# Performance work log

Hardware: AMD Instinct MI355X
Metric: run time of the kernel (lower is better)

## Reference

```python
import jax, jax.numpy as jnp
import numpy as np

C = 256
GROUPS = 32
HEADS = 4
EPS = 1e-5

def setup_inputs() -> dict:
    key = jax.random.key(0)
    ks = jax.random.split(key, 6)
    N, H, W = 4, 64, 64
    s = 1.0 / np.sqrt(C)
    return {
        "x": jax.random.normal(ks[0], (N, C, H, W), dtype=jnp.float32),
        "gamma": jnp.ones((C,), jnp.float32),
        "beta": jnp.zeros((C,), jnp.float32),
        "Wq": jax.random.normal(ks[1], (C, C), jnp.float32) * s,
        "Wk": jax.random.normal(ks[2], (C, C), jnp.float32) * s,
        "Wv": jax.random.normal(ks[3], (C, C), jnp.float32) * s,
        "Wp": jax.random.normal(ks[4], (C, C), jnp.float32) * s,
        "bp": jnp.zeros((C,), jnp.float32),
    }

def group_norm(x, gamma, beta):
    N, Cc, H, W = x.shape
    xg = x.reshape(N, GROUPS, Cc // GROUPS, H, W)
    mean = jnp.mean(xg, axis=(2, 3, 4), keepdims=True)
    var = jnp.var(xg, axis=(2, 3, 4), keepdims=True)
    xg = (xg - mean) * jax.lax.rsqrt(var + EPS)
    x = xg.reshape(N, Cc, H, W)
    return x * gamma[None, :, None, None] + beta[None, :, None, None]

def reference(x, gamma, beta, Wq, Wk, Wv, Wp, bp):
    N, Cc, H, W = x.shape
    dh = Cc // HEADS
    L = H * W
    xn = group_norm(x, gamma, beta)           # [N,C,H,W]
    xf = xn.reshape(N, Cc, L)                 # [N,C,L]
    # 1x1 convs == channel matmuls; split into heads: [N,heads,L,dh]
    def proj_heads(Wm):
        t = jnp.einsum('oc,ncl->nol', Wm, xf)
        return t.reshape(N, HEADS, dh, L).transpose(0, 1, 3, 2)
    q = proj_heads(Wq)
    k = proj_heads(Wk)
    v = proj_heads(Wv)
    scale = dh ** -0.5
    attn = jnp.einsum('nhld,nhmd->nhlm', q, k) * scale  # [N,heads,L,L]
    attn = jax.nn.softmax(attn, axis=-1)
    out = jnp.einsum('nhlm,nhmd->nhld', attn, v)        # [N,heads,L,dh]
    out = out.transpose(0, 1, 3, 2).reshape(N, Cc, L)   # [N,C,L]
    out = jnp.einsum('oc,ncl->nol', Wp, out) + bp[None, :, None]
    return out.reshape(N, Cc, H, W)
```

## Files before the change

kernel.cpp:

```cpp
#include <hip/hip_runtime.h>
#include <cstddef>
#include <cstdint>

#define NB 4
#define CC 256
#define LL 4096
#define NG 32
#define CPG 8
#define NH 4
#define DH 64
#define PSPLIT 4194304

static constexpr float EPSV  = 1e-5f;
static constexpr float SCALE_Q = 0.125f * 1.4426950408889634f;

typedef __attribute__((ext_vector_type(8))) short bf16x8;
typedef __attribute__((ext_vector_type(4))) float f32x4;
typedef _Float16 f16x8 __attribute__((ext_vector_type(8)));
typedef _Float16 f16x4 __attribute__((ext_vector_type(4)));
typedef __fp16  h16x2 __attribute__((ext_vector_type(2)));

__device__ __forceinline__ short f2bf(float f) {
  unsigned u = __float_as_uint(f);
  unsigned r = (u + 0x7fffu + ((u >> 16) & 1u)) >> 16;
  return (short)r;
}
__device__ __forceinline__ short f2h(float f) {
  union { _Float16 h; short s; } u;
  u.h = (_Float16)f;
  return u.s;
}
__device__ __forceinline__ int sw(int row, int chunk) {
  return row * 64 + ((chunk ^ (row & 7)) * 8);
}

__global__ __launch_bounds__(256) void gnstats_wcvt(
    const float* __restrict__ x, float* __restrict__ pstat,
    const float* __restrict__ Wq, const float* __restrict__ Wk,
    const float* __restrict__ Wv, const float* __restrict__ Wp,
    short* __restrict__ wdst) {
  __shared__ float r1[4], r2[4];
  const int blk = blockIdx.x;
  if (blk < 512) {
    const int grp = blk >> 2, qtr = blk & 3;
    const float* xp = x + (size_t)grp * CPG * LL + qtr * 1024 + threadIdx.x * 4;
    float s = 0.f, ss = 0.f;
    #pragma unroll
    for (int cc = 0; cc < 8; ++cc) {
      const float4 v = *(const float4*)(xp + (size_t)cc * LL);
      s  += v.x + v.y + v.z + v.w;
      ss += v.x * v.x + v.y * v.y + v.z * v.z + v.w * v.w;
    }
    #pragma unroll
    for (int off = 32; off; off >>= 1) {
      s  += __shfl_down(s, off);
      ss += __shfl_down(ss, off);
    }
    const int wid = threadIdx.x >> 6, lane = threadIdx.x & 63;
    if (lane == 0) { r1[wid] = s; r2[wid] = ss; }
    __syncthreads();
    if (threadIdx.x == 0) {
      float S = 0.f, SS = 0.f;
      #pragma unroll
      for (int w = 0; w < 4; ++w) { S += r1[w]; SS += r2[w]; }
      pstat[blk * 2]     = S;
      pstat[blk * 2 + 1] = SS;
    }
  } else {
    const int wblk = blk - 512;
    const int which = wblk >> 5;
    const float* src = (which == 0) ? Wq : (which == 1) ? Wk : (which == 2) ? Wv : Wp;
    const int base = (wblk & 31) * 2048 + threadIdx.x * 8;
    const float4 v0 = *(const float4*)(src + base);
    const float4 v1 = *(const float4*)(src + base + 4);
    short ob[8] __attribute__((aligned(16)));
    if (which < 3) {
      ob[0] = f2bf(v0.x); ob[1] = f2bf(v0.y); ob[2] = f2bf(v0.z); ob[3] = f2bf(v0.w);
      ob[4] = f2bf(v1.x); ob[5] = f2bf(v1.y); ob[6] = f2bf(v1.z); ob[7] = f2bf(v1.w);
    } else {
      ob[0] = f2h(v0.x); ob[1] = f2h(v0.y); ob[2] = f2h(v0.z); ob[3] = f2h(v0.w);
      ob[4] = f2h(v1.x); ob[5] = f2h(v1.y); ob[6] = f2h(v1.z); ob[7] = f2h(v1.w);
    }
    const int o = base >> 8, c = base & 255;
    const int dst = (((o >> 4) * 8 + (c >> 5)) * 64 + ((c >> 3) & 3) * 16 + (o & 15)) * 8;
    *(uint4*)(wdst + which * 65536 + dst) = *(const uint4*)ob;
  }
}

__global__ __launch_bounds__(256) void qkv_gemm(
    const float* __restrict__ x, const float* __restrict__ gamma,
    const float* __restrict__ beta, const float* __restrict__ pstat,
    const short* __restrict__ Wqb, const short* __restrict__ Wkb,
    const short* __restrict__ Wvb,
    short* __restrict__ Qt, short* __restrict__ Kt, _Float16* __restrict__ Vo) {
  __shared__ __align__(16) short smem[64 * 136];
  const int lt = blockIdx.y, ot2 = blockIdx.x;
  const int n = lt >> 7, l0 = (lt & 127) << 5;
  const int wave = threadIdx.x >> 6, lane = threadIdx.x & 63;
  const int lq = lane & 15, quad = lane >> 4;

  {
    const int cc = threadIdx.x >> 3, l8 = threadIdx.x & 7;
    const int grp = n * NG + cc;
    float S = 0.f, SS = 0.f;
    #pragma unroll
    for (int w = 0; w < 4; ++w) {
      S  += pstat[(grp * 4 + w) * 2];
      SS += pstat[(grp * 4 + w) * 2 + 1];
    }
    const float mean = S / 32768.f;
    const float rstd = rsqrtf(SS / 32768.f - mean * mean + EPSV);
    const float* xp = x + (size_t)(n * CC + cc * CPG) * LL + l0 + l8 * 4;
    short ob[4][8] __attribute__((aligned(16)));
    #pragma unroll
    for (int j = 0; j < 8; ++j) {
      const float scl = rstd * gamma[cc * CPG + j];
      const float shf = beta[cc * CPG + j] - mean * scl;
      const float4 v = *(const float4*)(xp + (size_t)j * LL);
      ob[0][j] = f2bf(v.x * scl + shf);
      ob[1][j] = f2bf(v.y * scl + shf);
      ob[2][j] = f2bf(v.z * scl + shf);
      ob[3][j] = f2bf(v.w * scl + shf);
    }
    short* dst = smem + (l8 * 4) * 264 + cc * 8;
    #pragma unroll
    for (int jj = 0; jj < 4; ++jj)
      *(uint4*)(dst + jj * 264) = *(const uint4*)ob[jj];
  }
  __syncthreads();

  const int tb   = (ot2 * 8 + wave) * 8;
  const int loff = lane * 8;
  const short* xl = smem + lq * 264 + quad * 8;

  const f32x4 z = {0.f, 0.f, 0.f, 0.f};
  f32x4 aq[2][2] = {{z, z}, {z, z}};
  f32x4 ak[2][2] = {{z, z}, {z, z}};
  f32x4 av[2][2] = {{z, z}, {z, z}};

  #pragma unroll
  for (int c5 = 0; c5 < 8; ++c5) {
    const int c0 = c5 * 32;
    const bf16x8 fq0 = *(const bf16x8*)(Wqb + (tb + c5) * 512 + loff);
    const bf16x8 fq1 = *(const bf16x8*)(Wqb + (tb + 32 + c5) * 512 + loff);
    const bf16x8 fk0 = *(const bf16x8*)(Wkb + (tb + c5) * 512 + loff);
    const bf16x8 fk1 = *(const bf16x8*)(Wkb + (tb + 32 + c5) * 512 + loff);
    const bf16x8 fv0 = *(const bf16x8*)(Wvb + (tb + c5) * 512 + loff);
    const bf16x8 fv1 = *(const bf16x8*)(Wvb + (tb + 32 + c5) * 512 + loff);
    #pragma unroll
    for (int n0 = 0; n0 < 2; ++n0) {
      const bf16x8 fb = *(const bf16x8*)(xl + (n0 * 16) * 264 + c0);
      aq[0][n0] = __builtin_amdgcn_mfma_f32_16x16x32_bf16(fq0, fb, aq[0][n0], 0, 0, 0);
      aq[1][n0] = __builtin_amdgcn_mfma_f32_16x16x32_bf16(fq1, fb, aq[1][n0], 0, 0, 0);
      ak[0][n0] = __builtin_amdgcn_mfma_f32_16x16x32_bf16(fk0, fb, ak[0][n0], 0, 0, 0);
      ak[1][n0] = __builtin_amdgcn_mfma_f32_16x16x32_bf16(fk1, fb, ak[1][n0], 0, 0, 0);
      av[0][n0] = __builtin_amdgcn_mfma_f32_16x16x32_bf16(fv0, fb, av[0][n0], 0, 0, 0);
      av[1][n0] = __builtin_amdgcn_mfma_f32_16x16x32_bf16(fv1, fb, av[1][n0], 0, 0, 0);
    }
  }

  #pragma unroll
  for (int w = 0; w < 2; ++w) {
    const size_t hb = (size_t)(n * NH + ot2 * 2 + w);
    #pragma unroll
    for (int n0 = 0; n0 < 2; ++n0) {
      const int pos = l0 + 8 * (lq >> 2) + 4 * n0 + (lq & 3);
      #pragma unroll
      for (int r = 0; r < 4; ++r)
        Vo[(hb * DH + wave * 16 + quad * 4 + r) * LL + pos] = (_Float16)av[w][n0][r];
    }
  }

  __syncthreads();
  short* qt_l = smem;
  short* kt_l = smem + 32 * 136;
  #pragma unroll
  for (int w = 0; w < 2; ++w)
    #pragma unroll
    for (int n0 = 0; n0 < 2; ++n0)
      #pragma unroll
      for (int r = 0; r < 4; ++r) {
        const int row = n0 * 16 + lq;
        const int col = w * 64 + wave * 16 + quad * 4 + r;
        qt_l[row * 136 + col] = f2bf(aq[w][n0][r] * SCALE_Q);
        kt_l[row * 136 + col] = f2bf(ak[w][n0][r]);
      }
  __syncthreads();
  #pragma unroll
  for (int i = 0; i < 2; ++i) {
    const int u = threadIdx.x + i * 256;
    const int row = u >> 4, ch16 = u & 15;
    const int h = ot2 * 2 + (ch16 >> 3);
    const int d0 = (ch16 & 7) * 8;
    const size_t hb = (size_t)(n * NH + h);
    *(uint4*)(Qt + (hb * LL + l0 + row) * DH + d0) = *(const uint4*)&qt_l[row * 136 + ch16 * 8];
    *(uint4*)(Kt + (hb * LL + l0 + row) * DH + d0) = *(const uint4*)&kt_l[row * 136 + ch16 * 8];
  }
}

__global__ __launch_bounds__(256, 2) void attn_mfma_kernel(
    const short* __restrict__ Qt, const short* __restrict__ Kt,
    const _Float16* __restrict__ Vb, _Float16* __restrict__ Opart,
    float* __restrict__ lpart) {
  __shared__ __align__(16) short    k_lds[2][64 * 64];
  __shared__ __align__(16) _Float16 v_lds[2][64 * 64];

  const int t = threadIdx.x;
  const int wave = t >> 6, lane = t & 63;
  const int lq = lane & 15, quad = lane >> 4;
  const int l0 = blockIdx.x * 256;
  const int h = blockIdx.y >> 1, split = blockIdx.y & 1;
  const int n = blockIdx.z;
  const int kbase = split * 2048;
  const int R = n * NH + h;
  const size_t hb = (size_t)R * (size_t)LL * DH;
  const short* const Kp = Kt + hb;
  const _Float16* const Vp = Vb + hb;

  const int qbase = l0 + wave * 64;
  bf16x8 qb[4][2];
  #pragma unroll
  for (int qf = 0; qf < 4; ++qf)
    #pragma unroll
    for (int c = 0; c < 2; ++c)
      qb[qf][c] = *(const bf16x8*)(Qt + hb + (size_t)(qbase + qf * 16 + lq) * DH + c * 32 + quad * 8);

  const f32x4 z = {0.f, 0.f, 0.f, 0.f};
  f32x4 o[4][4] = {{z, z, z, z}, {z, z, z, z}, {z, z, z, z}, {z, z, z, z}};
  f32x4 ol[4] = {z, z, z, z};

  f16x8 ones8;
  #pragma unroll
  for (int i = 0; i < 8; ++i) ones8[i] = (_Float16)1.0f;

  const int srow = t >> 3, sch = t & 7;

  {
    *(uint4*)&k_lds[0][sw(srow, sch)]      = *(const uint4*)(Kp + (size_t)(kbase + srow) * DH + sch * 8);
    *(uint4*)&k_lds[0][sw(32 + srow, sch)] = *(const uint4*)(Kp + (size_t)(kbase + 32 + srow) * DH + sch * 8);
    *(uint4*)&v_lds[0][sw(srow, sch)]      = *(const uint4*)(Vp + (size_t)srow * LL + kbase + sch * 8);
    *(uint4*)&v_lds[0][sw(32 + srow, sch)] = *(const uint4*)(Vp + (size_t)(32 + srow) * LL + kbase + sch * 8);
  }
  __syncthreads();

  for (int kt = 0; kt < 32; ++kt) {
    const int cur = kt & 1;
    uint4 kpre[2], vpre[2];
    if (kt < 31) {
      const int kpos = kbase + (kt + 1) * 64;
      kpre[0] = *(const uint4*)(Kp + (size_t)(kpos + srow) * DH + sch * 8);
      kpre[1] = *(const uint4*)(Kp + (size_t)(kpos + 32 + srow) * DH + sch * 8);
      vpre[0] = *(const uint4*)(Vp + (size_t)srow * LL + kpos + sch * 8);
      vpre[1] = *(const uint4*)(Vp + (size_t)(32 + srow) * LL + kpos + sch * 8);
    }
    const short* kb = k_lds[cur];
    const _Float16* vbuf = v_lds[cur];

    union PU { f16x4 h4[2]; f16x8 h8; } af[2][4];
    #pragma unroll
    for (int mf = 0; mf < 4; ++mf) {
      const bf16x8 ka0 = *(const bf16x8*)&kb[sw(mf * 16 + lq, quad)];
      const bf16x8 ka1 = *(const bf16x8*)&kb[sw(mf * 16 + lq, 4 + quad)];
      #pragma unroll
      for (int qf = 0; qf < 4; ++qf) {
        f32x4 zz = {0.f, 0.f, 0.f, 0.f};
        zz = __builtin_amdgcn_mfma_f32_16x16x32_bf16(ka0, qb[qf][0], zz, 0, 0, 0);
        zz = __builtin_amdgcn_mfma_f32_16x16x32_bf16(ka1, qb[qf][1], zz, 0, 0, 0);
        union { h16x2 h2[2]; f16x4 h4; } u;
        u.h2[0] = __builtin_amdgcn_cvt_pkrtz(__builtin_amdgcn_exp2f(zz[0]),
                                             __builtin_amdgcn_exp2f(zz[1]));
        u.h2[1] = __builtin_amdgcn_cvt_pkrtz(__builtin_amdgcn_exp2f(zz[2]),
                                             __builtin_amdgcn_exp2f(zz[3]));
        af[mf >> 1][qf].h4[mf & 1] = u.h4;
      }
    }

    #pragma unroll
    for (int qf = 0; qf < 4; ++qf) {
      ol[qf] = __builtin_amdgcn_mfma_f32_16x16x32_f16(af[0][qf].h8, ones8, ol[qf], 0, 0, 0);
      ol[qf] = __builtin_amdgcn_mfma_f32_16x16x32_f16(af[1][qf].h8, ones8, ol[qf], 0, 0, 0);
    }

    #pragma unroll
    for (int df = 0; df < 4; ++df)
      #pragma unroll
      for (int cc = 0; cc < 2; ++cc) {
        const f16x8 vb8 = *(const f16x8*)&vbuf[sw(df * 16 + lq, cc * 4 + quad)];
        #pragma unroll
        for (int qf = 0; qf < 4; ++qf)
          o[qf][df] = __builtin_amdgcn_mfma_f32_16x16x32_f16(af[cc][qf].h8, vb8, o[qf][df], 0, 0, 0);
      }

    if (kt < 31) {
      const int nxt = 1 - cur;
      *(uint4*)&k_lds[nxt][sw(srow, sch)]      = kpre[0];
      *(uint4*)&k_lds[nxt][sw(32 + srow, sch)] = kpre[1];
      *(uint4*)&v_lds[nxt][sw(srow, sch)]      = vpre[0];
      *(uint4*)&v_lds[nxt][sw(32 + srow, sch)] = vpre[1];
      __syncthreads();
    }
  }

  const size_t pb = ((size_t)split * 16 + R) * (size_t)LL * DH;
  #pragma unroll
  for (int qf = 0; qf < 4; ++qf) {
    if (lq == 0) {
      #pragma unroll
      for (int r = 0; r < 4; ++r)
        lpart[((size_t)split * 16 + R) * LL + qbase + qf * 16 + quad * 4 + r] = ol[qf][r];
    }
    #pragma unroll
    for (int df = 0; df < 4; ++df)
      #pragma unroll
      for (int r = 0; r < 4; ++r) {
        const int q = qbase + qf * 16 + quad * 4 + r;
        Opart[pb + (size_t)q * DH + df * 16 + lq] = (_Float16)o[qf][df][r];
      }
  }
}

__global__ __launch_bounds__(256) void proj_gemm(
    const _Float16* __restrict__ Opart, const float* __restrict__ lpart,
    const _Float16* __restrict__ Wpf, const float* __restrict__ bp,
    float* __restrict__ out) {
  __shared__ __align__(16) _Float16 fb_lds[2][32 * 64];
  const int lt = blockIdx.y, ot2 = blockIdx.x;
  const int n = lt >> 7, l0 = (lt & 127) << 5;
  const int wave = threadIdx.x >> 6, lane = threadIdx.x & 63;
  const int lq = lane & 15, quad = lane >> 4;
  const int t = threadIdx.x;
  const int qr = t >> 3, ch = t & 7;

  const int tb   = (ot2 * 8 + wave) * 8;
  const int loff = lane * 8;

  auto stage_load = [&](int h, f16x8& dst) {
    const _Float16* Op = Opart + ((size_t)(n * NH + h) * LL + l0) * DH;
    const size_t rr = (size_t)(n * NH + h) * LL + l0 + qr;
    const _Float16 il = (_Float16)(1.0f / (lpart[rr] + lpart[rr + 16 * (size_t)LL]));
    const size_t e = (size_t)qr * DH + ch * 8;
    const f16x8 b0 = *(const f16x8*)(Op + e);
    const f16x8 b1 = *(const f16x8*)(Op + e + (size_t)PSPLIT);
    f16x8 sc8;
    #pragma unroll
    for (int i = 0; i < 8; ++i) sc8[i] = il;
    dst = (b0 + b1) * sc8;
  };

  {
    f16x8 f0;
    stage_load(0, f0);
    *(f16x8*)&fb_lds[0][sw(qr, ch)] = f0;
  }
  __syncthreads();

  const f32x4 z = {0.f, 0.f, 0.f, 0.f};
  f32x4 acc[2][2] = {{z, z}, {z, z}};
  for (int h = 0; h < NH; ++h) {
    const int cur = h & 1;
    f16x8 pre;
    if (h < NH - 1) stage_load(h + 1, pre);
    #pragma unroll
    for (int cw = 0; cw < 2; ++cw) {
      const int c5 = 2 * h + cw;
      const int c_idx = cw * 4 + quad;
      const f16x8 fa0 = *(const f16x8*)(Wpf + (tb + c5) * 512 + loff);
      const f16x8 fa1 = *(const f16x8*)(Wpf + (tb + 32 + c5) * 512 + loff);
      #pragma unroll
      for (int n0 = 0; n0 < 2; ++n0) {
        const f16x8 fb = *(const f16x8*)&fb_lds[cur][sw(n0 * 16 + lq, c_idx)];
        acc[0][n0] = __builtin_amdgcn_mfma_f32_16x16x32_f16(fa0, fb, acc[0][n0], 0, 0, 0);
        acc[1][n0] = __builtin_amdgcn_mfma_f32_16x16x32_f16(fa1, fb, acc[1][n0], 0, 0, 0);
      }
    }
    if (h < NH - 1) {
      *(f16x8*)&fb_lds[cur ^ 1][sw(qr, ch)] = pre;
      __syncthreads();
    }
  }

  #pragma unroll
  for (int w = 0; w < 2; ++w)
    #pragma unroll
    for (int r = 0; r < 4; ++r) {
      const int oo = ot2 * 128 + w * 64 + wave * 16 + quad * 4 + r;
      const float bias = bp[oo];
      #pragma unroll
      for (int n0 = 0; n0 < 2; ++n0)
        out[((size_t)n * CC + oo) * LL + l0 + n0 * 16 + lq] = acc[w][n0][r] + bias;
    }
}

extern "C" void kernel_launch(void* const* d_in, const int* in_sizes, int n_in,
                              void* d_out, int out_size, void* d_ws, size_t ws_size,
                              hipStream_t stream) {
  const float* x     = (const float*)d_in[0];
  const float* gamma = (const float*)d_in[1];
  const float* beta  = (const float*)d_in[2];
  const float* Wq    = (const float*)d_in[3];
  const float* Wk    = (const float*)d_in[4];
  const float* Wv    = (const float*)d_in[5];
  const float* Wp    = (const float*)d_in[6];
  const float* bp    = (const float*)d_in[7];
  float* out = (float*)d_out;

  const size_t S = (size_t)NB * CC * LL;
  short*     Qt  = (short*)d_ws;
  short*     Kt  = Qt + S;
  _Float16*  Vo  = (_Float16*)(Kt + S);
  short*     Wb  = (short*)(Vo + S);
  _Float16*  Opart = (_Float16*)(Wb + 4 * 65536);
  float*     lpart = (float*)(Opart + 2 * (size_t)PSPLIT);
  float*     pstat = lpart + 2 * 16 * (size_t)LL;

  gnstats_wcvt<<<640,                 256, 0, stream>>>(x, pstat, Wq, Wk, Wv, Wp, Wb);
  qkv_gemm   <<<dim3(2, 512),         256, 0, stream>>>(x, gamma, beta, pstat,
                 Wb, Wb + 65536, Wb + 131072, Qt, Kt, Vo);
  attn_mfma_kernel<<<dim3(LL/256, NH*2, NB), 256, 0, stream>>>(Qt, Kt, Vo, Opart, lpart);
  proj_gemm  <<<dim3(2, 512),         256, 0, stream>>>(Opart, lpart,
                 (const _Float16*)(Wb + 196608), bp, out);
}
```

Measured before the change: 172.3 us.

## Write fp16 transposed copy of x in stats kernel for QKV GEMM

The group-norm statistics kernel, which already reads all of x, now also writes an fp16 copy transposed to [N, L, C]. The QKV GEMM then reads that half-precision, channel-contiguous copy instead of strided fp32 x, applies the normalization and stages it into shared memory. This halves the bytes the GEMM reads for x and makes its loads contiguous across channels. In exchange the stats kernel writes an extra 8 MB with scattered 16-byte stores, and the extra fp16 rounding of x before normalization adds some error.

New measurement: 173.6 us. No clear change (+0.8%).

```diff
diff --git a/kernel.cpp b/kernel.cpp
--- a/kernel.cpp
+++ b/kernel.cpp
@@ -36,6 +36,7 @@
 
 __global__ __launch_bounds__(256) void gnstats_wcvt(
     const float* __restrict__ x, float* __restrict__ pstat,
+    _Float16* __restrict__ xT,
     const float* __restrict__ Wq, const float* __restrict__ Wk,
     const float* __restrict__ Wv, const float* __restrict__ Wp,
     short* __restrict__ wdst) {
@@ -43,14 +44,22 @@
   const int blk = blockIdx.x;
   if (blk < 512) {
     const int grp = blk >> 2, qtr = blk & 3;
+    const int n = grp >> 5, g = grp & 31;
     const float* xp = x + (size_t)grp * CPG * LL + qtr * 1024 + threadIdx.x * 4;
     float s = 0.f, ss = 0.f;
+    short ob[4][8] __attribute__((aligned(16)));
     #pragma unroll
     for (int cc = 0; cc < 8; ++cc) {
       const float4 v = *(const float4*)(xp + (size_t)cc * LL);
       s  += v.x + v.y + v.z + v.w;
       ss += v.x * v.x + v.y * v.y + v.z * v.z + v.w * v.w;
-    }
+      ob[0][cc] = f2h(v.x); ob[1][cc] = f2h(v.y);
+      ob[2][cc] = f2h(v.z); ob[3][cc] = f2h(v.w);
+    }
+    _Float16* op = xT + ((size_t)n * LL + qtr * 1024 + threadIdx.x * 4) * CC + g * CPG;
+    #pragma unroll
+    for (int j = 0; j < 4; ++j)
+      *(uint4*)(op + (size_t)j * CC) = *(const uint4*)ob[j];
     #pragma unroll
     for (int off = 32; off; off >>= 1) {
       s  += __shfl_down(s, off);
@@ -88,7 +97,7 @@
 }
 
 __global__ __launch_bounds__(256) void qkv_gemm(
-    const float* __restrict__ x, const float* __restrict__ gamma,
+    const _Float16* __restrict__ xT, const float* __restrict__ gamma,
     const float* __restrict__ beta, const float* __restrict__ pstat,
     const short* __restrict__ Wqb, const short* __restrict__ Wkb,
     const short* __restrict__ Wvb,
@@ -100,8 +109,9 @@
   const int lq = lane & 15, quad = lane >> 4;
 
   {
-    const int cc = threadIdx.x >> 3, l8 = threadIdx.x & 7;
-    const int grp = n * NG + cc;
+    const int ch = threadIdx.x & 31;
+    const int r0 = threadIdx.x >> 5;
+    const int grp = n * NG + ch;
     float S = 0.f, SS = 0.f;
     #pragma unroll
     for (int w = 0; w < 4; ++w) {
@@ -110,22 +120,22 @@
     }
     const float mean = S / 32768.f;
     const float rstd = rsqrtf(SS / 32768.f - mean * mean + EPSV);
-    const float* xp = x + (size_t)(n * CC + cc * CPG) * LL + l0 + l8 * 4;
-    short ob[4][8] __attribute__((aligned(16)));
+    float scl[8], shf[8];
     #pragma unroll
     for (int j = 0; j < 8; ++j) {
-      const float scl = rstd * gamma[cc * CPG + j];
-      const float shf = beta[cc * CPG + j] - mean * scl;
-      const float4 v = *(const float4*)(xp + (size_t)j * LL);
-      ob[0][j] = f2bf(v.x * scl + shf);
-      ob[1][j] = f2bf(v.y * scl + shf);
-      ob[2][j] = f2bf(v.z * scl + shf);
-      ob[3][j] = f2bf(v.w * scl + shf);
-    }
-    short* dst = smem + (l8 * 4) * 264 + cc * 8;
-    #pragma unroll
-    for (int jj = 0; jj < 4; ++jj)
-      *(uint4*)(dst + jj * 264) = *(const uint4*)ob[jj];
+      scl[j] = rstd * gamma[ch * CPG + j];
+      shf[j] = beta[ch * CPG + j] - mean * scl[j];
+    }
+    #pragma unroll
+    for (int j = 0; j < 4; ++j) {
+      const int row = r0 + 8 * j;
+      const f16x8 v = *(const f16x8*)(xT + ((size_t)(n * LL + l0 + row)) * CC + ch * 8);
+      short ob[8] __attribute__((aligned(16)));
+      #pragma unroll
+      for (int e = 0; e < 8; ++e)
+        ob[e] = f2bf((float)v[e] * scl[e] + shf[e]);
+      *(uint4*)(smem + row * 264 + ch * 8) = *(const uint4*)ob;
+    }
   }
   __syncthreads();
 
@@ -412,9 +422,10 @@
   _Float16*  Opart = (_Float16*)(Wb + 4 * 65536);
   float*     lpart = (float*)(Opart + 2 * (size_t)PSPLIT);
   float*     pstat = lpart + 2 * 16 * (size_t)LL;
-
-  gnstats_wcvt<<<640,                 256, 0, stream>>>(x, pstat, Wq, Wk, Wv, Wp, Wb);
-  qkv_gemm   <<<dim3(2, 512),         256, 0, stream>>>(x, gamma, beta, pstat,
+  _Float16*  xT    = (_Float16*)(pstat + 1024);
+
+  gnstats_wcvt<<<640,                 256, 0, stream>>>(x, pstat, xT, Wq, Wk, Wv, Wp, Wb);
+  qkv_gemm   <<<dim3(2, 512),         256, 0, stream>>>(xT, gamma, beta, pstat,
                  Wb, Wb + 65536, Wb + 131072, Qt, Kt, Vo);
   attn_mfma_kernel<<<dim3(LL/256, NH*2, NB), 256, 0, stream>>>(Qt, Kt, Vo, Opart, lpart);
   proj_gemm  <<<dim3(2, 512),         256, 0, stream>>>(Opart, lpart,
```
